# Kernel optimization log

Hardware: AMD Instinct MI355X
Metric: run time of the kernel (lower is better)

The kernel has to match this reference:

```python
import jax, jax.numpy as jnp
import numpy as np
import math

HIDDEN = 1024
N_HEADS = 16
HEAD_DIM = HIDDEN // N_HEADS
N_BLOCKS = 16
BATCH = 2
SEQ = 4096


def setup_inputs() -> dict:
    key = jax.random.key(0)
    ks = jax.random.split(key, 8)
    attention_input = jax.random.normal(ks[0], (BATCH, SEQ, HIDDEN), dtype=jnp.float32)
    attention_mask = jnp.ones((BATCH, SEQ), dtype=jnp.float32)
    # permutation over the num_blocks*num_heads flattened (block, head) axis
    permutation = jax.random.permutation(ks[1], N_BLOCKS * N_HEADS)
    init = 0.02
    q_w = jax.random.normal(ks[2], (HIDDEN, N_HEADS, HEAD_DIM), dtype=jnp.float32) * init
    q_b = jax.random.normal(ks[3], (N_HEADS, HEAD_DIM), dtype=jnp.float32) * init
    k_w = jax.random.normal(ks[4], (HIDDEN, N_HEADS, HEAD_DIM), dtype=jnp.float32) * init
    k_b = jax.random.normal(ks[5], (N_HEADS, HEAD_DIM), dtype=jnp.float32) * init
    v_w = jax.random.normal(ks[6], (HIDDEN, N_HEADS, HEAD_DIM), dtype=jnp.float32) * init
    v_b = jax.random.normal(ks[7], (N_HEADS, HEAD_DIM), dtype=jnp.float32) * init
    return {"attention_input": attention_input, "attention_mask": attention_mask,
            "permutation": permutation, "q_w": q_w, "q_b": q_b,
            "k_w": k_w, "k_b": k_b, "v_w": v_w, "v_b": v_b}


def reference(attention_input, attention_mask, permutation, q_w, q_b, k_w, k_b, v_w, v_b):
    B = attention_mask.shape[0]
    S = attention_mask.shape[1]
    nb = N_BLOCKS
    nh, d = q_b.shape
    blk = S // nb
    # QKV projections: [B,S,H] x [H,N,D] -> [B,S,N,D]
    q = jnp.einsum('bsh,hnd->bsnd', attention_input, q_w) + q_b
    k = jnp.einsum('bsh,hnd->bsnd', attention_input, k_w) + k_b
    v = jnp.einsum('bsh,hnd->bsnd', attention_input, v_w) + v_b

    def blockify(x):  # [B,S,N,D] -> [B, nb, nh, blk, d]
        return x.reshape(B, nb, blk, nh, d).transpose(0, 1, 3, 2, 4)

    q = blockify(q)
    # flatten (block, head) axis and gather per permutation
    k = blockify(k).reshape(B, nb * nh, blk, d)[:, permutation].reshape(B, nb, nh, blk, d)
    v = blockify(v).reshape(B, nb * nh, blk, d)[:, permutation].reshape(B, nb, nh, blk, d)

    scale = 1.0 / math.sqrt(float(d))
    logits = jnp.einsum('bgnqd,bgnkd->bgnqk', q, k) * scale  # block-local scores
    attn = jax.nn.softmax(logits, axis=-1)  # dropout prob 0 / eval mode
    ctx = jnp.einsum('bgnqk,bgnkd->bgnqd', attn, v)
    # [B,nb,nh,blk,d] -> [B,nb,blk,nh,d] -> [B,S,nh,d]
    return ctx.transpose(0, 1, 3, 2, 4).reshape(B, S, nh, d)
```

## Files before the change

kernel.cpp:

```cpp
#include <hip/hip_runtime.h>
#include <hip/hip_bf16.h>
#include <stdint.h>

typedef __attribute__((ext_vector_type(4))) float f32x4;
typedef __attribute__((ext_vector_type(8))) short s16x8;

__device__ inline short f2bf(float f) {
  union { float f; uint32_t u; } v; v.f = f;
  uint32_t r = v.u + 0x7fffu + ((v.u >> 16) & 1u);
  return (short)(r >> 16);
}

__device__ inline void gload_lds16(const void* g, void* l) {
  __builtin_amdgcn_global_load_lds((const __attribute__((address_space(1))) void*)g,
                                   (__attribute__((address_space(3))) void*)l,
                                   16, 0, 0);
}

#define MFMA16 __builtin_amdgcn_mfma_f32_16x16x32_bf16

__device__ inline uint32_t lds_off(const void* p) {
  return (uint32_t)(uintptr_t)(const __attribute__((address_space(3))) char*)p;
}
__device__ inline s16x8 dsr_b128(uint32_t addr) {
  s16x8 r;
  asm volatile("ds_read_b128 %0, %1" : "=v"(r) : "v"(addr));
  return r;
}

__global__ __launch_bounds__(256) void k_convert_x(const float* __restrict__ x,
                                                   short* __restrict__ xb) {
  int i = (blockIdx.x * 256 + threadIdx.x) * 8;
  const float4* p = (const float4*)(x + i);
  float4 a = p[0], b = p[1];
  s16x8 o;
  o[0] = f2bf(a.x); o[1] = f2bf(a.y); o[2] = f2bf(a.z); o[3] = f2bf(a.w);
  o[4] = f2bf(b.x); o[5] = f2bf(b.y); o[6] = f2bf(b.z); o[7] = f2bf(b.w);
  *(s16x8*)(xb + i) = o;
}

__global__ __launch_bounds__(256) void k_transpose_w(const float* __restrict__ qw,
                                                     const float* __restrict__ kw,
                                                     const float* __restrict__ vw,
                                                     short* __restrict__ wt) {
  __shared__ float tile[64][65];
  int a  = blockIdx.x >> 8;
  int t2 = blockIdx.x & 255;
  int k0 = (t2 >> 4) << 6;
  int n0 = (t2 & 15) << 6;
  const float* w = (a == 0) ? qw : (a == 1) ? kw : vw;
  int c = threadIdx.x & 63, rr = threadIdx.x >> 6;
#pragma unroll
  for (int i = 0; i < 16; ++i) {
    int r = i * 4 + rr;
    tile[r][c] = w[(k0 + r) * 1024 + n0 + c];
  }
  __syncthreads();
  short* o = wt + a * 1048576;
#pragma unroll
  for (int i = 0; i < 16; ++i) {
    int r = i * 4 + rr;
    o[(n0 + r) * 1024 + k0 + c] = f2bf(tile[c][r]);
  }
}

__global__ __launch_bounds__(512, 2) void k_gemm(const short* __restrict__ xb,
                                                 const short* __restrict__ wt,
                                                 const float* __restrict__ bias3,
                                                 short* __restrict__ C) {
  __shared__ short lds[73728];
  const int tid = threadIdx.x, lane = tid & 63, wv = tid >> 6;
  const int wm = wv >> 2, wn = wv & 3;
  int wg = blockIdx.x;
  wg = (wg & 7) * 64 + (wg >> 3);
  const int mt = wg >> 4, nt = wg & 15;
  const short* asrc = xb + (size_t)(mt * 256) * 1024;
  const short* bsrc = wt + (size_t)(nt * 192) * 1024;

  int srcA[4], srcB[3];
#pragma unroll
  for (int i = 0; i < 4; ++i) {
    int c = i * 512 + tid, r = c >> 3, ss = c & 7;
    srcA[i] = r * 1024 + (ss ^ (r & 7)) * 8;
  }
#pragma unroll
  for (int i = 0; i < 3; ++i) {
    int c = i * 512 + tid, r = c >> 3, ss = c & 7;
    srcB[i] = r * 1024 + (ss ^ (r & 7)) * 8;
  }

  const uint32_t ldsb = lds_off(lds);
  const uint32_t slot0 = ((uint32_t)((lane >> 4) ^ (lane & 7))) << 4;
  const uint32_t Ab0 = ldsb + (uint32_t)(wm * 128 + (lane & 15)) * 128 + slot0;
  const uint32_t Ab1 = Ab0 ^ 64;
  const uint32_t Bb0 = ldsb + 98304 + (uint32_t)(wn * 48 + (lane & 15)) * 128 + slot0;
  const uint32_t Bb1 = Bb0 ^ 64;

  f32x4 acc[8][3] = {};

  auto STAGE_A = [&](int t, int slot) {
    const short* at = asrc + t * 64;
    char* l = (char*)lds + slot * 32768;
#pragma unroll
    for (int i = 0; i < 4; ++i) gload_lds16(at + srcA[i], l + (i * 512 + tid) * 16);
  };
  auto STAGE_B = [&](int t, int slot) {
    const short* bt = bsrc + t * 64;
    char* l = (char*)lds + 98304 + slot * 24576;
#pragma unroll
    for (int i = 0; i < 3; ++i) gload_lds16(bt + srcB[i], l + (i * 512 + tid) * 16);
  };

  auto COMPUTE = [&](int i) {
    const uint32_t aS = (uint32_t)((i % 3) * 32768), bS = (uint32_t)((i & 1) * 24576);
    const uint32_t a0 = Ab0 + aS, a1 = Ab1 + aS, b0 = Bb0 + bS, b1 = Bb1 + bS;
    s16x8 af[4][2], bf[3][2];
#pragma unroll
    for (int n = 0; n < 3; ++n) {
      bf[n][0] = dsr_b128(b0 + n * 2048);
      bf[n][1] = dsr_b128(b1 + n * 2048);
    }
#pragma unroll
    for (int m = 0; m < 4; ++m) {
      af[m][0] = dsr_b128(a0 + m * 2048);
      af[m][1] = dsr_b128(a1 + m * 2048);
    }
    asm volatile("s_waitcnt lgkmcnt(0)" ::: "memory");
    __builtin_amdgcn_sched_barrier(0);
    __builtin_amdgcn_s_setprio(1);
#pragma unroll
    for (int ks = 0; ks < 2; ++ks)
#pragma unroll
      for (int m = 0; m < 4; ++m)
#pragma unroll
        for (int n = 0; n < 3; ++n)
          acc[m][n] = MFMA16(af[m][ks], bf[n][ks], acc[m][n], 0, 0, 0);
    __builtin_amdgcn_s_setprio(0);
    __builtin_amdgcn_sched_barrier(0);
#pragma unroll
    for (int m = 0; m < 4; ++m) {
      af[m][0] = dsr_b128(a0 + (m + 4) * 2048);
      af[m][1] = dsr_b128(a1 + (m + 4) * 2048);
    }
    asm volatile("s_waitcnt lgkmcnt(0)" ::: "memory");
    __builtin_amdgcn_sched_barrier(0);
    __builtin_amdgcn_s_setprio(1);
#pragma unroll
    for (int ks = 0; ks < 2; ++ks)
#pragma unroll
      for (int m = 0; m < 4; ++m)
#pragma unroll
        for (int n = 0; n < 3; ++n)
          acc[m + 4][n] = MFMA16(af[m][ks], bf[n][ks], acc[m + 4][n], 0, 0, 0);
    __builtin_amdgcn_s_setprio(0);
  };

  STAGE_B(0, 0);
  STAGE_A(0, 0);
  STAGE_A(1, 1);

  for (int i = 0; i < 15; ++i) {
    asm volatile("s_waitcnt vmcnt(4)" ::: "memory");
    __builtin_amdgcn_s_barrier();
    __builtin_amdgcn_sched_barrier(0);
    STAGE_B(i + 1, (i + 1) & 1);
    if (i < 14) STAGE_A(i + 2, (i + 2) % 3);
    COMPUTE(i);
  }
  asm volatile("s_waitcnt vmcnt(0)" ::: "memory");
  __builtin_amdgcn_s_barrier();
  __builtin_amdgcn_sched_barrier(0);
  COMPUTE(15);

  int nbase = nt * 192 + wn * 48;
  int mbase = mt * 256 + wm * 128;
#pragma unroll
  for (int n = 0; n < 3; ++n) {
    int col = nbase + n * 16 + (lane & 15);
    float bv = bias3[col];
#pragma unroll
    for (int m = 0; m < 8; ++m)
#pragma unroll
      for (int r = 0; r < 4; ++r) {
        int mm = mbase + m * 16 + ((lane >> 4) << 2) + r;
        C[(size_t)mm * 3072 + col] = f2bf(acc[m][n][r] + bv);
      }
  }
}

__global__ __launch_bounds__(512) void k_attn(const short* __restrict__ QKV,
                                              const int* __restrict__ perm,
                                              float* __restrict__ out) {
  __shared__ short Qs[256 * 64];
  __shared__ short Ks[256 * 64];
  __shared__ short Vs[64 * 256];
  __shared__ short Ps[8 * 1024];

  int tid = threadIdx.x;
  int lane = tid & 63, wv = tid >> 6;
  int bx = blockIdx.x;
  int b = bx >> 8, g = (bx >> 4) & 15, n = bx & 15;
  int p = perm[g * 16 + n];
  int pg = p >> 4, ph = p & 15;

  const short* qsrc = QKV + (size_t)(b * 4096 + g * 256) * 3072 + n * 64;
  const short* ksrc = QKV + (size_t)(b * 4096 + pg * 256) * 3072 + 1024 + ph * 64;
  const short* vsrc = QKV + (size_t)(b * 4096 + pg * 256) * 3072 + 2048 + ph * 64;

  s16x8 vreg[4];
#pragma unroll
  for (int i = 0; i < 4; ++i) {
    int c = i * 512 + tid;
    int t = c >> 3;
    int d0 = (c & 7) << 3;
    vreg[i] = *(const s16x8*)(vsrc + t * 3072 + d0);
  }
#pragma unroll
  for (int i = 0; i < 4; ++i) {
    int c = i * 512 + tid;
    int row = c >> 3;
    int colb = (c & 7) << 4;
    int sc = colb ^ ((row & 7) << 4);
    gload_lds16(qsrc + row * 3072 + (sc >> 1), (char*)Qs + c * 16);
    gload_lds16(ksrc + row * 3072 + (sc >> 1), (char*)Ks + c * 16);
  }
#pragma unroll
  for (int i = 0; i < 4; ++i) {
    int c = i * 512 + tid;
    int t = c >> 3;
    int d0 = (c & 7) << 3;
#pragma unroll
    for (int j = 0; j < 8; ++j) {
      int d = d0 + j;
      int sl = (d & 7) ^ ((d >> 3) & 7);
      int by = d * 512 + ((t * 2) ^ (sl << 4));
      *(short*)((char*)Vs + by) = vreg[i][j];
    }
  }
  __syncthreads();

  int qr0 = wv * 32;
  f32x4 accS[2][16] = {};
#pragma unroll
  for (int ks = 0; ks < 2; ++ks) {
    int cb = (ks << 6) + ((lane >> 4) << 4);
    s16x8 aq[2];
#pragma unroll
    for (int rf = 0; rf < 2; ++rf) {
      int row = qr0 + rf * 16 + (lane & 15);
      aq[rf] = *(const s16x8*)((const char*)Qs + row * 128 + (cb ^ ((row & 7) << 4)));
    }
#pragma unroll
    for (int cf = 0; cf < 16; ++cf) {
      int row = cf * 16 + (lane & 15);
      s16x8 bk = *(const s16x8*)((const char*)Ks + row * 128 + (cb ^ ((row & 7) << 4)));
      accS[0][cf] = MFMA16(aq[0], bk, accS[0][cf], 0, 0, 0);
      accS[1][cf] = MFMA16(aq[1], bk, accS[1][cf], 0, 0, 0);
    }
  }

  const float sc_log2e = 0.125f * 1.44269504088896f;
  float mx[2][4], inv[2][4];
#pragma unroll
  for (int rf = 0; rf < 2; ++rf)
#pragma unroll
    for (int r = 0; r < 4; ++r) {
      float m_ = accS[rf][0][r];
#pragma unroll
      for (int cf = 1; cf < 16; ++cf) m_ = fmaxf(m_, accS[rf][cf][r]);
#pragma unroll
      for (int msk = 1; msk < 16; msk <<= 1) m_ = fmaxf(m_, __shfl_xor(m_, msk));
      mx[rf][r] = m_;
    }
#pragma unroll
  for (int rf = 0; rf < 2; ++rf)
#pragma unroll
    for (int r = 0; r < 4; ++r) {
      float s_ = 0.f;
#pragma unroll
      for (int cf = 0; cf < 16; ++cf) {
        float e = exp2f((accS[rf][cf][r] - mx[rf][r]) * sc_log2e);
        accS[rf][cf][r] = e;
        s_ += e;
      }
#pragma unroll
      for (int msk = 1; msk < 16; msk <<= 1) s_ += __shfl_xor(s_, msk);
      inv[rf][r] = 1.0f / s_;
    }

  f32x4 accO[2][4] = {};
  short* pchunk = Ps + wv * 1024;
#pragma unroll
  for (int ks = 0; ks < 8; ++ks) {
#pragma unroll
    for (int rf = 0; rf < 2; ++rf)
#pragma unroll
      for (int half = 0; half < 2; ++half) {
        int cf = ks * 2 + half;
        int kvl = half * 16 + (lane & 15);
        int qp = (lane >> 4) << 2;
        int base = rf * 512 + ((kvl >> 3) << 7) + (kvl & 7);
#pragma unroll
        for (int r = 0; r < 4; ++r)
          pchunk[base + (qp + r) * 8] = f2bf(accS[rf][cf][r]);
      }
    int cbv = (ks << 6) + ((lane >> 4) << 4);
#pragma unroll
    for (int rf = 0; rf < 2; ++rf) {
      s16x8 ap = *(const s16x8*)(pchunk + rf * 512 + lane * 8);
#pragma unroll
      for (int dc = 0; dc < 4; ++dc) {
        int vrow = dc * 16 + (lane & 15);
        int sl = (vrow & 7) ^ ((vrow >> 3) & 7);
        s16x8 bv = *(const s16x8*)((const char*)Vs + vrow * 512 + (cbv ^ (sl << 4)));
        accO[rf][dc] = MFMA16(ap, bv, accO[rf][dc], 0, 0, 0);
      }
    }
  }

#pragma unroll
  for (int rf = 0; rf < 2; ++rf)
#pragma unroll
    for (int dc = 0; dc < 4; ++dc)
#pragma unroll
      for (int r = 0; r < 4; ++r) {
        int q = qr0 + rf * 16 + ((lane >> 4) << 2) + r;
        int d = dc * 16 + (lane & 15);
        out[(size_t)((b * 4096 + g * 256 + q) * 16 + n) * 64 + d] = accO[rf][dc][r] * inv[rf][r];
      }
}

extern "C" void kernel_launch(void* const* d_in, const int* in_sizes, int n_in,
                              void* d_out, int out_size, void* d_ws, size_t ws_size,
                              hipStream_t stream) {
  const float* x    = (const float*)d_in[0];
  const int*   perm = (const int*)d_in[2];
  const float* qw   = (const float*)d_in[3];
  const float* qb   = (const float*)d_in[4];
  const float* kw   = (const float*)d_in[5];
  const float* kb   = (const float*)d_in[6];
  const float* vw   = (const float*)d_in[7];
  const float* vb   = (const float*)d_in[8];
  float* out = (float*)d_out;

  char* ws = (char*)d_ws;
  short* Xb    = (short*)(ws);
  short* Wt    = (short*)(ws + 16777216UL);
  short* C     = (short*)(ws + 23068672UL);
  float* bias3 = (float*)(ws + 73400320UL);

  hipMemcpyAsync(bias3,        qb, 4096, hipMemcpyDeviceToDevice, stream);
  hipMemcpyAsync(bias3 + 1024, kb, 4096, hipMemcpyDeviceToDevice, stream);
  hipMemcpyAsync(bias3 + 2048, vb, 4096, hipMemcpyDeviceToDevice, stream);

  k_convert_x<<<4096, 256, 0, stream>>>(x, Xb);
  k_transpose_w<<<768, 256, 0, stream>>>(qw, kw, vw, Wt);
  k_gemm<<<512, 512, 0, stream>>>(Xb, Wt, bias3, C);
  k_attn<<<512, 512, 0, stream>>>(C, perm, out);
}
```

Before: 119.1 us.

## Split GEMM k-tile into four barrier-separated phases interleaving loads and MFMAs

Restructures the QKV projection GEMM main loop so each k-tile runs as four phases. Each phase issues a small LDS fragment read plus part of the next global-to-LDS prefetch, then runs a block of MFMAs at raised priority. The A-tile prefetch is split into halves so global loads spread across phases instead of bursting at the start of each tile. This halves the fragment registers in flight and aims to overlap memory traffic with matrix math more evenly. The cost is several extra workgroup barriers per k-tile, and the vmcnt accounting becomes more delicate.

New measurement: 120.6 us. About the same (+1.2%).

```diff
diff --git a/kernel.cpp b/kernel.cpp
--- a/kernel.cpp
+++ b/kernel.cpp
@@ -98,11 +98,12 @@
 
   f32x4 acc[8][3] = {};
 
-  auto STAGE_A = [&](int t, int slot) {
+  auto STAGE_A2 = [&](int t, int slot, int half) {
     const short* at = asrc + t * 64;
     char* l = (char*)lds + slot * 32768;
 #pragma unroll
-    for (int i = 0; i < 4; ++i) gload_lds16(at + srcA[i], l + (i * 512 + tid) * 16);
+    for (int i = half * 2; i < half * 2 + 2; ++i)
+      gload_lds16(at + srcA[i], l + (i * 512 + tid) * 16);
   };
   auto STAGE_B = [&](int t, int slot) {
     const short* bt = bsrc + t * 64;
@@ -111,66 +112,85 @@
     for (int i = 0; i < 3; ++i) gload_lds16(bt + srcB[i], l + (i * 512 + tid) * 16);
   };
 
-  auto COMPUTE = [&](int i) {
-    const uint32_t aS = (uint32_t)((i % 3) * 32768), bS = (uint32_t)((i & 1) * 24576);
-    const uint32_t a0 = Ab0 + aS, a1 = Ab1 + aS, b0 = Bb0 + bS, b1 = Bb1 + bS;
-    s16x8 af[4][2], bf[3][2];
-#pragma unroll
-    for (int n = 0; n < 3; ++n) {
-      bf[n][0] = dsr_b128(b0 + n * 2048);
-      bf[n][1] = dsr_b128(b1 + n * 2048);
-    }
-#pragma unroll
-    for (int m = 0; m < 4; ++m) {
-      af[m][0] = dsr_b128(a0 + m * 2048);
-      af[m][1] = dsr_b128(a1 + m * 2048);
-    }
+  STAGE_B(0, 0);
+  STAGE_A2(0, 0, 0); STAGE_A2(0, 0, 1);
+  STAGE_A2(1, 1, 0); STAGE_A2(1, 1, 1);
+  asm volatile("s_waitcnt vmcnt(4)" ::: "memory");
+  __builtin_amdgcn_s_barrier();
+
+  for (int kt = 0; kt < 16; ++kt) {
+    const uint32_t aS = (uint32_t)((kt % 3) * 32768);
+    const uint32_t bS = (uint32_t)((kt & 1) * 24576);
+    const uint32_t a0 = Ab0 + aS, a1 = Ab1 + aS;
+    const uint32_t b0 = Bb0 + bS, b1 = Bb1 + bS;
+    s16x8 af[4], bf[3];
+
+    bf[0] = dsr_b128(b0); bf[1] = dsr_b128(b0 + 2048); bf[2] = dsr_b128(b0 + 4096);
+    af[0] = dsr_b128(a0); af[1] = dsr_b128(a0 + 2048);
+    af[2] = dsr_b128(a0 + 4096); af[3] = dsr_b128(a0 + 6144);
+    if (kt < 15) STAGE_B(kt + 1, (kt + 1) & 1);
+    __builtin_amdgcn_s_barrier();
     asm volatile("s_waitcnt lgkmcnt(0)" ::: "memory");
     __builtin_amdgcn_sched_barrier(0);
     __builtin_amdgcn_s_setprio(1);
 #pragma unroll
-    for (int ks = 0; ks < 2; ++ks)
-#pragma unroll
-      for (int m = 0; m < 4; ++m)
-#pragma unroll
-        for (int n = 0; n < 3; ++n)
-          acc[m][n] = MFMA16(af[m][ks], bf[n][ks], acc[m][n], 0, 0, 0);
+    for (int m = 0; m < 4; ++m)
+#pragma unroll
+      for (int n = 0; n < 3; ++n)
+        acc[m][n] = MFMA16(af[m], bf[n], acc[m][n], 0, 0, 0);
     __builtin_amdgcn_s_setprio(0);
-    __builtin_amdgcn_sched_barrier(0);
-#pragma unroll
-    for (int m = 0; m < 4; ++m) {
-      af[m][0] = dsr_b128(a0 + (m + 4) * 2048);
-      af[m][1] = dsr_b128(a1 + (m + 4) * 2048);
-    }
+    __builtin_amdgcn_s_barrier();
+
+    af[0] = dsr_b128(a0 + 8192);  af[1] = dsr_b128(a0 + 10240);
+    af[2] = dsr_b128(a0 + 12288); af[3] = dsr_b128(a0 + 14336);
+    if (kt < 14) STAGE_A2(kt + 2, (kt + 2) % 3, 0);
+    __builtin_amdgcn_s_barrier();
     asm volatile("s_waitcnt lgkmcnt(0)" ::: "memory");
     __builtin_amdgcn_sched_barrier(0);
     __builtin_amdgcn_s_setprio(1);
 #pragma unroll
-    for (int ks = 0; ks < 2; ++ks)
-#pragma unroll
-      for (int m = 0; m < 4; ++m)
-#pragma unroll
-        for (int n = 0; n < 3; ++n)
-          acc[m + 4][n] = MFMA16(af[m][ks], bf[n][ks], acc[m + 4][n], 0, 0, 0);
+    for (int m = 0; m < 4; ++m)
+#pragma unroll
+      for (int n = 0; n < 3; ++n)
+        acc[m + 4][n] = MFMA16(af[m], bf[n], acc[m + 4][n], 0, 0, 0);
     __builtin_amdgcn_s_setprio(0);
-  };
-
-  STAGE_B(0, 0);
-  STAGE_A(0, 0);
-  STAGE_A(1, 1);
-
-  for (int i = 0; i < 15; ++i) {
-    asm volatile("s_waitcnt vmcnt(4)" ::: "memory");
-    __builtin_amdgcn_s_barrier();
+    __builtin_amdgcn_s_barrier();
+
+    bf[0] = dsr_b128(b1); bf[1] = dsr_b128(b1 + 2048); bf[2] = dsr_b128(b1 + 4096);
+    af[0] = dsr_b128(a1); af[1] = dsr_b128(a1 + 2048);
+    af[2] = dsr_b128(a1 + 4096); af[3] = dsr_b128(a1 + 6144);
+    if (kt < 14) STAGE_A2(kt + 2, (kt + 2) % 3, 1);
+    __builtin_amdgcn_s_barrier();
+    asm volatile("s_waitcnt lgkmcnt(0)" ::: "memory");
     __builtin_amdgcn_sched_barrier(0);
-    STAGE_B(i + 1, (i + 1) & 1);
-    if (i < 14) STAGE_A(i + 2, (i + 2) % 3);
-    COMPUTE(i);
-  }
-  asm volatile("s_waitcnt vmcnt(0)" ::: "memory");
-  __builtin_amdgcn_s_barrier();
-  __builtin_amdgcn_sched_barrier(0);
-  COMPUTE(15);
+    __builtin_amdgcn_s_setprio(1);
+#pragma unroll
+    for (int m = 0; m < 4; ++m)
+#pragma unroll
+      for (int n = 0; n < 3; ++n)
+        acc[m][n] = MFMA16(af[m], bf[n], acc[m][n], 0, 0, 0);
+    __builtin_amdgcn_s_setprio(0);
+    __builtin_amdgcn_s_barrier();
+
+    af[0] = dsr_b128(a1 + 8192);  af[1] = dsr_b128(a1 + 10240);
+    af[2] = dsr_b128(a1 + 12288); af[3] = dsr_b128(a1 + 14336);
+    __builtin_amdgcn_s_barrier();
+    asm volatile("s_waitcnt lgkmcnt(0)" ::: "memory");
+    __builtin_amdgcn_sched_barrier(0);
+    __builtin_amdgcn_s_setprio(1);
+#pragma unroll
+    for (int m = 0; m < 4; ++m)
+#pragma unroll
+      for (int n = 0; n < 3; ++n)
+        acc[m + 4][n] = MFMA16(af[m], bf[n], acc[m + 4][n], 0, 0, 0);
+    __builtin_amdgcn_s_setprio(0);
+    if (kt < 14) {
+      asm volatile("s_waitcnt vmcnt(4)" ::: "memory");
+    } else if (kt == 14) {
+      asm volatile("s_waitcnt vmcnt(0)" ::: "memory");
+    }
+    __builtin_amdgcn_s_barrier();
+  }
 
   int nbase = nt * 192 + wn * 48;
   int mbase = mt * 256 + wm * 128;
```
